# Kernel optimization log

Hardware: AMD Instinct MI355X
Metric: run time of the kernel (lower is better)

## Reference

```python
import jax, jax.numpy as jnp
import numpy as np

N = 50000
E = 800000
IN_FEATS = 128
OUT_FEATS = 16
EDGE_FEATS = 1
NUM_HEADS = 8


def setup_inputs() -> dict:
    key = jax.random.key(0)
    ks = jax.random.split(key, 8)

    def xavier(k, shape):
        fan_in, fan_out = shape[-1], shape[-2] if len(shape) > 1 else shape[-1]
        bound = float(np.sqrt(6.0 / (shape[0] + shape[1])))
        return jax.random.uniform(k, shape, jnp.float32, -bound, bound)

    h = jax.random.normal(ks[0], (N, IN_FEATS), jnp.float32)
    edge_index = jax.random.randint(ks[1], (2, E), 0, N, jnp.int32)
    edge_feat = jax.random.normal(ks[2], (E, EDGE_FEATS), jnp.float32)
    # W_node stored as [in_feats, out_feats*num_heads] so h @ W_node == torch Linear(h)
    W_node = xavier(ks[3], (IN_FEATS, OUT_FEATS * NUM_HEADS))
    W_edge = xavier(ks[4], (EDGE_FEATS, NUM_HEADS))
    a_src = xavier(ks[5], (NUM_HEADS, OUT_FEATS))
    a_dst = xavier(ks[6], (NUM_HEADS, OUT_FEATS))
    return {"h": h, "edge_index": edge_index, "edge_feat": edge_feat,
            "W_node": W_node, "W_edge": W_edge, "a_src": a_src, "a_dst": a_dst}


def reference(h, edge_index, edge_feat, W_node, W_edge, a_src, a_dst):
    n = h.shape[0]
    src, dst = edge_index[0], edge_index[1]
    # node projection: [N, H, F]
    h_trans = (h @ W_node).reshape(n, NUM_HEADS, OUT_FEATS)
    # edge projection: [E, H]
    e_trans = edge_feat @ W_edge
    src_feat = h_trans[src]  # [E, H, F]
    dst_feat = h_trans[dst]  # [E, H, F]
    attn = (src_feat * a_src).sum(-1) + (dst_feat * a_dst).sum(-1) + e_trans  # [E, H]
    attn = jax.nn.leaky_relu(attn, negative_slope=0.2)
    # segment softmax over edges grouped by dst
    max_val = jax.ops.segment_max(attn, dst, num_segments=n)  # [N, H]
    exp_attn = jnp.exp(attn - max_val[dst])
    sum_exp = jax.ops.segment_sum(exp_attn, dst, num_segments=n)  # [N, H]
    alpha = exp_attn / jnp.maximum(sum_exp[dst], 1e-12)  # [E, H]
    msg = src_feat * alpha[..., None]  # [E, H, F]
    out = jax.ops.segment_sum(msg, dst, num_segments=n)  # [N, H, F]
    return out.mean(axis=1)  # [N, F]
```

## Files before the change

kernel.cpp:

```cpp
#include <hip/hip_runtime.h>

#define N_NODES 50000
#define N_EDGES 800000
#define IN_F    128
#define HEADS   8
#define OUT_F   16
#define NB_PROJ 782
#define NB_HIST 3125

typedef unsigned short u16;
typedef __attribute__((ext_vector_type(8))) short bf16x8;
typedef __attribute__((ext_vector_type(4))) float f32x4;

__device__ __forceinline__ float bf2f(u16 u) {
    return __uint_as_float(((unsigned)u) << 16);
}
__device__ __forceinline__ u16 f2bf(float f) {
    unsigned u = __float_as_uint(f);
    unsigned r = 0x7fffu + ((u >> 16) & 1u);
    return (u16)((u + r) >> 16);
}
__device__ __forceinline__ float ldf(const void* p, int i, bool bf) {
    return bf ? bf2f(((const u16*)p)[i]) : ((const float*)p)[i];
}

__global__ void probe_dtype(const void* __restrict__ h, int* __restrict__ flag) {
    if (threadIdx.x == 0 && blockIdx.x == 0) {
        const u16* u = (const u16*)h;
        int cnt = 0;
        for (int i = 0; i < 128; ++i) {
            int e = (u[i] >> 7) & 0xFF;
            if (e >= 90 && e <= 141) cnt++;
        }
        *flag = (cnt >= 110) ? 1 : 0;
    }
}

#define WT_STRIDE 136
__global__ __launch_bounds__(256) void proj_hist(
    const void* __restrict__ h, const void* __restrict__ Wn,
    const void* __restrict__ a_srcp, const void* __restrict__ a_dstp,
    const int* __restrict__ flag, const int* __restrict__ ei,
    u16* __restrict__ ht, float* __restrict__ s_src, float* __restrict__ s_dst,
    int* __restrict__ deg, int* __restrict__ rank)
{
    if (blockIdx.x >= NB_PROJ) {
        int e = (blockIdx.x - NB_PROJ) * 256 + threadIdx.x;
        if (e < N_EDGES) rank[e] = atomicAdd(&deg[ei[N_EDGES + e]], 1);
        return;
    }

    const bool bf = (*flag) != 0;
    __shared__ u16 Wsh[IN_F * WT_STRIDE];
    __shared__ float a_sh[2][IN_F];
    const int tid = threadIdx.x;

    if (tid < 128) a_sh[0][tid] = ldf(a_srcp, tid, bf);
    else           a_sh[1][tid - 128] = ldf(a_dstp, tid - 128, bf);

    {
        const int c8  = (tid & 15) * 8;
        const int kof = tid >> 4;
        const int ksw = (tid & 7) << 3;
        bf16x8 wv[8];
        if (bf) {
            const u16* wp = (const u16*)Wn;
            #pragma unroll
            for (int j = 0; j < 8; ++j)
                wv[j] = *(const bf16x8*)(wp + (size_t)(j * 16 + kof) * IN_F + c8);
        } else {
            const float* wp = (const float*)Wn;
            #pragma unroll
            for (int j = 0; j < 8; ++j) {
                const float* rp = wp + (size_t)(j * 16 + kof) * IN_F + c8;
                float4 fa = *(const float4*)(rp);
                float4 fb = *(const float4*)(rp + 4);
                bf16x8 t;
                t[0] = (short)f2bf(fa.x); t[1] = (short)f2bf(fa.y);
                t[2] = (short)f2bf(fa.z); t[3] = (short)f2bf(fa.w);
                t[4] = (short)f2bf(fb.x); t[5] = (short)f2bf(fb.y);
                t[6] = (short)f2bf(fb.z); t[7] = (short)f2bf(fb.w);
                wv[j] = t;
            }
        }
        #pragma unroll
        for (int j = 0; j < 8; ++j) {
            int kk = (j * 16 + kof) ^ ksw;
            #pragma unroll
            for (int jj = 0; jj < 8; ++jj)
                Wsh[(c8 + jj) * WT_STRIDE + kk] = (u16)wv[j][jj];
        }
    }
    __syncthreads();

    const int wave = tid >> 6, lane = tid & 63;
    const int m = lane & 15, q = lane >> 4;
    const int row_t = blockIdx.x * 64 + wave * 16;

    bf16x8 afr[4];
    int arow = row_t + m;
    if (arow >= N_NODES) arow = N_NODES - 1;
    if (bf) {
        const u16* hp = (const u16*)h + (size_t)arow * IN_F;
        #pragma unroll
        for (int kt = 0; kt < 4; ++kt)
            afr[kt] = *(const bf16x8*)(hp + kt * 32 + q * 8);
    } else {
        const float* hp = (const float*)h + (size_t)arow * IN_F;
        #pragma unroll
        for (int kt = 0; kt < 4; ++kt) {
            bf16x8 t;
            #pragma unroll
            for (int j = 0; j < 8; ++j) t[j] = (short)f2bf(hp[kt * 32 + q * 8 + j]);
            afr[kt] = t;
        }
    }

    f32x4 accs[8];
    #pragma unroll
    for (int ct = 0; ct < 8; ++ct) {
        const int csw = ((2 * ct + (m >> 3)) & 7) << 3;
        f32x4 acc = {0.f, 0.f, 0.f, 0.f};
        #pragma unroll
        for (int kt = 0; kt < 4; ++kt) {
            bf16x8 bfr = *(const bf16x8*)(Wsh + (ct * 16 + m) * WT_STRIDE
                                          + ((kt * 32 + q * 8) ^ csw));
            acc = __builtin_amdgcn_mfma_f32_16x16x32_bf16(afr[kt], bfr, acc, 0, 0, 0);
        }
        accs[ct] = acc;
    }

    __syncthreads();

    const int wbase = wave * 16;
    #pragma unroll
    for (int ct = 0; ct < 8; ++ct)
        #pragma unroll
        for (int r = 0; r < 4; ++r)
            Wsh[(wbase + q * 4 + r) * WT_STRIDE + ct * 16 + m] = f2bf(accs[ct][r]);

    const int r2 = lane & 15, hp2 = lane >> 4;
    const int grow = row_t + r2;
    const u16* wrow = Wsh + (wbase + r2) * WT_STRIDE;
    bf16x8 h0 = *(const bf16x8*)(wrow + hp2 * 32);
    bf16x8 h1 = *(const bf16x8*)(wrow + hp2 * 32 + 8);
    bf16x8 h2 = *(const bf16x8*)(wrow + hp2 * 32 + 16);
    bf16x8 h3 = *(const bf16x8*)(wrow + hp2 * 32 + 24);

    if (grow < N_NODES) {
        u16* hb = ht + (size_t)grow * IN_F + hp2 * 32;
        *(bf16x8*)(hb)      = h0;
        *(bf16x8*)(hb + 8)  = h1;
        *(bf16x8*)(hb + 16) = h2;
        *(bf16x8*)(hb + 24) = h3;
    }

    #pragma unroll
    for (int hh = 0; hh < 2; ++hh) {
        const int hd = hp2 * 2 + hh;
        float s1 = 0.f, s2 = 0.f;
        #pragma unroll
        for (int f = 0; f < 8; ++f) {
            float xa = bf2f((u16)((hh == 0) ? h0[f] : h2[f]));
            float xb = bf2f((u16)((hh == 0) ? h1[f] : h3[f]));
            s1 = fmaf(xa, a_sh[0][hd * 16 + f], s1);
            s1 = fmaf(xb, a_sh[0][hd * 16 + 8 + f], s1);
            s2 = fmaf(xa, a_sh[1][hd * 16 + f], s2);
            s2 = fmaf(xb, a_sh[1][hd * 16 + 8 + f], s2);
        }
        if (grow < N_NODES) {
            s_src[grow * HEADS + hd] = s1;
            s_dst[grow * HEADS + hd] = s2;
        }
    }
}

__global__ __launch_bounds__(1024) void scan_deg(const int* __restrict__ deg,
                                                 int* __restrict__ csr) {
    __shared__ int wsums[16];
    const int tid = threadIdx.x, lane = tid & 63, wid = tid >> 6;
    const int base = tid * 52;

    int s = 0;
    for (int c = 0; c < 13; ++c) {
        int idx = base + c * 4;
        if (idx + 3 < N_NODES) {
            int4 q = *(const int4*)(deg + idx);
            s += q.x + q.y + q.z + q.w;
        } else {
            for (int j = 0; j < 4; ++j)
                if (idx + j < N_NODES) s += deg[idx + j];
        }
    }

    int x = s;
    #pragma unroll
    for (int o = 1; o < 64; o <<= 1) {
        int y = __shfl_up(x, o, 64);
        if (lane >= o) x += y;
    }
    if (lane == 63) wsums[wid] = x;
    __syncthreads();
    if (wid == 0) {
        int v = (lane < 16) ? wsums[lane] : 0;
        #pragma unroll
        for (int o = 1; o < 16; o <<= 1) {
            int y = __shfl_up(v, o, 16);
            if ((lane & 15) >= o) v += y;
        }
        if (lane < 16) wsums[lane] = v;
    }
    __syncthreads();
    int run = ((wid > 0) ? wsums[wid - 1] : 0) + (x - s);

    for (int c = 0; c < 13; ++c) {
        int idx = base + c * 4;
        if (idx + 3 < N_NODES) {
            int4 q = *(const int4*)(deg + idx);
            int4 o4 = {run, run + q.x, run + q.x + q.y, run + q.x + q.y + q.z};
            *(int4*)(csr + idx) = o4;
            run += q.x + q.y + q.z + q.w;
        } else {
            for (int j = 0; j < 4; ++j)
                if (idx + j < N_NODES) { csr[idx + j] = run; run += deg[idx + j]; }
        }
    }
    if (tid == 1023) csr[N_NODES] = run;
}

__global__ __launch_bounds__(256) void scatter_edges(
    const int* __restrict__ ei, const void* __restrict__ ef,
    const int* __restrict__ flag, const int* __restrict__ rank,
    const int* __restrict__ csr, int2* __restrict__ edges)
{
    const bool bf = (*flag) != 0;
    int e = blockIdx.x * 256 + threadIdx.x;
    if (e >= N_EDGES) return;
    int src = ei[e];
    int dst = ei[N_EDGES + e];
    int pos = csr[dst] + rank[e];
    float efv = ldf(ef, e, bf);
    edges[pos] = make_int2(src, __float_as_int(efv));
}

__global__ __launch_bounds__(256) void fused_aggregate(
    const int* __restrict__ csr, const int2* __restrict__ edges,
    const void* __restrict__ We,
    const float* __restrict__ s_src, const float* __restrict__ s_dst,
    const u16* __restrict__ ht, const int* __restrict__ flag,
    void* __restrict__ out)
{
    const bool bf = (*flag) != 0;
    int g = blockIdx.x * 32 + (threadIdx.x >> 3);
    if (g >= N_NODES) return;
    const int hd = threadIdx.x & 7;
    int beg = csr[g], end = csr[g + 1];
    const float dval = s_dst[g * HEADS + hd];
    const float wev = ldf(We, hd, bf);

    float num[16];
    #pragma unroll
    for (int f = 0; f < 16; ++f) num[f] = 0.f;
    float den = 0.f;

    int2 eN = make_int2(0, 0);
    float svN = 0.f;
    bf16x8 v0N = {0,0,0,0,0,0,0,0}, v1N = {0,0,0,0,0,0,0,0};
    if (beg < end) {
        eN = edges[beg];
        svN = s_src[eN.x * HEADS + hd];
        const u16* hp = ht + (size_t)eN.x * IN_F + hd * 16;
        v0N = *(const bf16x8*)hp;
        v1N = *(const bf16x8*)(hp + 8);
    }
    for (int i = beg; i < end; ++i) {
        int2 eC = eN;
        float sv = svN;
        bf16x8 v0 = v0N, v1 = v1N;
        if (i + 1 < end) {
            eN = edges[i + 1];
            svN = s_src[eN.x * HEADS + hd];
            const u16* hp = ht + (size_t)eN.x * IN_F + hd * 16;
            v0N = *(const bf16x8*)hp;
            v1N = *(const bf16x8*)(hp + 8);
        }
        float a = sv + dval + __int_as_float(eC.y) * wev;
        a = (a > 0.f) ? a : 0.2f * a;
        float ex = __expf(a);
        den += ex;
        #pragma unroll
        for (int f = 0; f < 8; ++f) {
            num[f]     = fmaf(ex, bf2f((u16)v0[f]), num[f]);
            num[8 + f] = fmaf(ex, bf2f((u16)v1[f]), num[8 + f]);
        }
    }

    float rc = 1.0f / fmaxf(den, 1e-12f);
    #pragma unroll
    for (int f = 0; f < 16; ++f) num[f] *= rc;
    #pragma unroll
    for (int o = 1; o < 8; o <<= 1)
        #pragma unroll
        for (int f = 0; f < 16; ++f)
            num[f] += __shfl_xor(num[f], o, 8);

    float o0 = num[2 * hd] * 0.125f;
    float o1 = num[2 * hd + 1] * 0.125f;
    if (bf) {
        unsigned pw = ((unsigned)f2bf(o1) << 16) | (unsigned)f2bf(o0);
        *(unsigned*)((u16*)out + (size_t)g * OUT_F + hd * 2) = pw;
    } else {
        float2 f2v = {o0, o1};
        *(float2*)((float*)out + (size_t)g * OUT_F + hd * 2) = f2v;
    }
}

extern "C" void kernel_launch(void* const* d_in, const int* in_sizes, int n_in,
                              void* d_out, int out_size, void* d_ws, size_t ws_size,
                              hipStream_t stream) {
    const void* h     = d_in[0];
    const int*  ei    = (const int*)d_in[1];
    const void* efeat = d_in[2];
    const void* Wn    = d_in[3];
    const void* We    = d_in[4];
    const void* a_src = d_in[5];
    const void* a_dst = d_in[6];

    char* ws = (char*)d_ws;
    int*   flag    = (int*)ws;   ws += 256;
    u16*   ht      = (u16*)ws;   ws += (size_t)N_NODES * IN_F * 2;
    float* s_src   = (float*)ws; ws += (size_t)N_NODES * HEADS * 4;
    float* s_dst   = (float*)ws; ws += (size_t)N_NODES * HEADS * 4;
    int*   deg     = (int*)ws;   ws += (size_t)50048 * 4;
    int*   csr     = (int*)ws;   ws += (size_t)50048 * 4;
    int*   rank    = (int*)ws;   ws += (size_t)N_EDGES * 4;
    int2*  edges   = (int2*)ws;  ws += (size_t)N_EDGES * 8;

    hipLaunchKernelGGL(probe_dtype, dim3(1), dim3(64), 0, stream, h, flag);
    hipMemsetAsync(deg, 0, (size_t)N_NODES * 4, stream);
    hipLaunchKernelGGL(proj_hist, dim3(NB_PROJ + NB_HIST), dim3(256),
                       0, stream, h, Wn, a_src, a_dst, flag, ei,
                       ht, s_src, s_dst, deg, rank);
    hipLaunchKernelGGL(scan_deg, dim3(1), dim3(1024), 0, stream, deg, csr);
    hipLaunchKernelGGL(scatter_edges, dim3((N_EDGES + 255) / 256), dim3(256),
                       0, stream, ei, efeat, flag, rank, csr, edges);
    hipLaunchKernelGGL(fused_aggregate, dim3((N_NODES + 31) / 32), dim3(256),
                       0, stream, csr, edges, We, s_src, s_dst, ht, flag, d_out);
}
```

Measured before the change: 213.1 us.

## Merge scan, scatter and aggregate into one cooperative kernel with grid syncs

Replaces the separate scan, scatter and aggregate kernels with a single cooperative kernel of 512 persistent blocks. Inside it, a two-level parallel scan builds the CSR offsets, then edges are scattered, then nodes are aggregated, with grid.sync between phases. The dtype probe kernel is dropped and each block now detects the dtype itself with a ballot. The aggregate loop is unrolled by four edges to raise the number of gather loads in flight. This removes several launches and the single-block serial scan, in exchange for grid-wide barriers and fewer resident blocks during the aggregation phase.

New measurement: 423.6 us. +98.8%, slower.

```diff
diff --git a/kernel.cpp b/kernel.cpp
--- a/kernel.cpp
+++ b/kernel.cpp
@@ -1,4 +1,7 @@
 #include <hip/hip_runtime.h>
+#include <hip/hip_cooperative_groups.h>
+
+namespace cg = cooperative_groups;
 
 #define N_NODES 50000
 #define N_EDGES 800000
@@ -7,6 +10,10 @@
 #define OUT_F   16
 #define NB_PROJ 782
 #define NB_HIST 3125
+#define NB2     512
+#define GSZ2    (NB2 * 256)
+#define CHUNK   98
+#define NBF     1563
 
 typedef unsigned short u16;
 typedef __attribute__((ext_vector_type(8))) short bf16x8;
@@ -24,23 +31,24 @@
     return bf ? bf2f(((const u16*)p)[i]) : ((const float*)p)[i];
 }
 
-__global__ void probe_dtype(const void* __restrict__ h, int* __restrict__ flag) {
-    if (threadIdx.x == 0 && blockIdx.x == 0) {
+__device__ __forceinline__ bool probe_bf(const void* h, int tid, int* bf_sh) {
+    if (tid < 64) {
         const u16* u = (const u16*)h;
-        int cnt = 0;
-        for (int i = 0; i < 128; ++i) {
-            int e = (u[i] >> 7) & 0xFF;
-            if (e >= 90 && e <= 141) cnt++;
-        }
-        *flag = (cnt >= 110) ? 1 : 0;
-    }
+        int e1 = (u[tid] >> 7) & 0xFF;
+        int e2 = (u[tid + 64] >> 7) & 0xFF;
+        unsigned long long b1 = __ballot(e1 >= 90 && e1 <= 141);
+        unsigned long long b2 = __ballot(e2 >= 90 && e2 <= 141);
+        if (tid == 0) *bf_sh = (__popcll(b1) + __popcll(b2) >= 110) ? 1 : 0;
+    }
+    __syncthreads();
+    return *bf_sh != 0;
 }
 
 #define WT_STRIDE 136
 __global__ __launch_bounds__(256) void proj_hist(
     const void* __restrict__ h, const void* __restrict__ Wn,
     const void* __restrict__ a_srcp, const void* __restrict__ a_dstp,
-    const int* __restrict__ flag, const int* __restrict__ ei,
+    const int* __restrict__ ei,
     u16* __restrict__ ht, float* __restrict__ s_src, float* __restrict__ s_dst,
     int* __restrict__ deg, int* __restrict__ rank)
 {
@@ -50,10 +58,11 @@
         return;
     }
 
-    const bool bf = (*flag) != 0;
     __shared__ u16 Wsh[IN_F * WT_STRIDE];
     __shared__ float a_sh[2][IN_F];
+    __shared__ int bf_sh;
     const int tid = threadIdx.x;
+    const bool bf = probe_bf(h, tid, &bf_sh);
 
     if (tid < 128) a_sh[0][tid] = ldf(a_srcp, tid, bf);
     else           a_sh[1][tid - 128] = ldf(a_dstp, tid - 128, bf);
@@ -91,7 +100,6 @@
                 Wsh[(c8 + jj) * WT_STRIDE + kk] = (u16)wv[j][jj];
         }
     }
-    __syncthreads();
 
     const int wave = tid >> 6, lane = tid & 63;
     const int m = lane & 15, q = lane >> 4;
@@ -115,6 +123,7 @@
             afr[kt] = t;
         }
     }
+    __syncthreads();
 
     f32x4 accs[8];
     #pragma unroll
@@ -129,7 +138,6 @@
         }
         accs[ct] = acc;
     }
-
     __syncthreads();
 
     const int wbase = wave * 16;
@@ -154,7 +162,6 @@
         *(bf16x8*)(hb + 16) = h2;
         *(bf16x8*)(hb + 24) = h3;
     }
-
     #pragma unroll
     for (int hh = 0; hh < 2; ++hh) {
         const int hd = hp2 * 2 + hh;
@@ -175,143 +182,173 @@
     }
 }
 
-__global__ __launch_bounds__(1024) void scan_deg(const int* __restrict__ deg,
-                                                 int* __restrict__ csr) {
-    __shared__ int wsums[16];
-    const int tid = threadIdx.x, lane = tid & 63, wid = tid >> 6;
-    const int base = tid * 52;
-
-    int s = 0;
-    for (int c = 0; c < 13; ++c) {
-        int idx = base + c * 4;
-        if (idx + 3 < N_NODES) {
-            int4 q = *(const int4*)(deg + idx);
-            s += q.x + q.y + q.z + q.w;
-        } else {
-            for (int j = 0; j < 4; ++j)
-                if (idx + j < N_NODES) s += deg[idx + j];
-        }
-    }
-
-    int x = s;
-    #pragma unroll
-    for (int o = 1; o < 64; o <<= 1) {
-        int y = __shfl_up(x, o, 64);
-        if (lane >= o) x += y;
-    }
-    if (lane == 63) wsums[wid] = x;
-    __syncthreads();
-    if (wid == 0) {
-        int v = (lane < 16) ? wsums[lane] : 0;
-        #pragma unroll
-        for (int o = 1; o < 16; o <<= 1) {
-            int y = __shfl_up(v, o, 16);
-            if ((lane & 15) >= o) v += y;
-        }
-        if (lane < 16) wsums[lane] = v;
-    }
-    __syncthreads();
-    int run = ((wid > 0) ? wsums[wid - 1] : 0) + (x - s);
-
-    for (int c = 0; c < 13; ++c) {
-        int idx = base + c * 4;
-        if (idx + 3 < N_NODES) {
-            int4 q = *(const int4*)(deg + idx);
-            int4 o4 = {run, run + q.x, run + q.x + q.y, run + q.x + q.y + q.z};
-            *(int4*)(csr + idx) = o4;
-            run += q.x + q.y + q.z + q.w;
-        } else {
-            for (int j = 0; j < 4; ++j)
-                if (idx + j < N_NODES) { csr[idx + j] = run; run += deg[idx + j]; }
-        }
-    }
-    if (tid == 1023) csr[N_NODES] = run;
-}
-
-__global__ __launch_bounds__(256) void scatter_edges(
-    const int* __restrict__ ei, const void* __restrict__ ef,
-    const int* __restrict__ flag, const int* __restrict__ rank,
-    const int* __restrict__ csr, int2* __restrict__ edges)
-{
-    const bool bf = (*flag) != 0;
-    int e = blockIdx.x * 256 + threadIdx.x;
-    if (e >= N_EDGES) return;
-    int src = ei[e];
-    int dst = ei[N_EDGES + e];
-    int pos = csr[dst] + rank[e];
-    float efv = ldf(ef, e, bf);
-    edges[pos] = make_int2(src, __float_as_int(efv));
-}
-
-__global__ __launch_bounds__(256) void fused_aggregate(
-    const int* __restrict__ csr, const int2* __restrict__ edges,
-    const void* __restrict__ We,
+__global__ __launch_bounds__(256, 2) void coop_tail(
+    const void* __restrict__ h, const int* __restrict__ ei,
+    const void* __restrict__ ef, const void* __restrict__ We,
     const float* __restrict__ s_src, const float* __restrict__ s_dst,
-    const u16* __restrict__ ht, const int* __restrict__ flag,
+    const u16* __restrict__ ht, const int* __restrict__ deg,
+    int* __restrict__ csr, const int* __restrict__ rank,
+    int* __restrict__ partials, int2* __restrict__ edges,
     void* __restrict__ out)
 {
-    const bool bf = (*flag) != 0;
-    int g = blockIdx.x * 32 + (threadIdx.x >> 3);
-    if (g >= N_NODES) return;
-    const int hd = threadIdx.x & 7;
-    int beg = csr[g], end = csr[g + 1];
-    const float dval = s_dst[g * HEADS + hd];
+    cg::grid_group grid = cg::this_grid();
+    __shared__ int wsums[8];
+    __shared__ int bf_sh;
+    const int tid = threadIdx.x, bid = blockIdx.x;
+    const int gtid = bid * 256 + tid;
+    const int lane = tid & 63, wid = tid >> 6;
+    const bool bf = probe_bf(h, tid, &bf_sh);
+
+    {
+        int idx = bid * CHUNK + tid;
+        int v = (tid < CHUNK && idx < N_NODES) ? deg[idx] : 0;
+        #pragma unroll
+        for (int o = 32; o > 0; o >>= 1) v += __shfl_xor(v, o, 64);
+        if (lane == 0) wsums[wid] = v;
+        __syncthreads();
+        if (tid == 0) partials[bid] = wsums[0] + wsums[1] + wsums[2] + wsums[3];
+    }
+    if (gtid == 0) csr[N_NODES] = N_EDGES;
+    grid.sync();
+
+    if (bid == 0) {
+        int p0 = 0, p1 = 0, p2 = 0, p3 = 0, s = 0;
+        if (tid < 128) {
+            p0 = partials[tid * 4];     p1 = partials[tid * 4 + 1];
+            p2 = partials[tid * 4 + 2]; p3 = partials[tid * 4 + 3];
+            s = p0 + p1 + p2 + p3;
+        }
+        int x = s;
+        #pragma unroll
+        for (int o = 1; o < 64; o <<= 1) {
+            int y = __shfl_up(x, o, 64);
+            if (lane >= o) x += y;
+        }
+        if (lane == 63) wsums[wid] = x;
+        __syncthreads();
+        if (tid == 0) { int t0 = wsums[0]; wsums[0] = 0; wsums[1] = t0; }
+        __syncthreads();
+        if (tid < 128) {
+            int run = wsums[wid] + (x - s);
+            partials[tid * 4]     = run; run += p0;
+            partials[tid * 4 + 1] = run; run += p1;
+            partials[tid * 4 + 2] = run; run += p2;
+            partials[tid * 4 + 3] = run;
+        }
+    }
+    grid.sync();
+
+    {
+        int idx = bid * CHUNK + tid;
+        int v = (tid < CHUNK && idx < N_NODES) ? deg[idx] : 0;
+        int x = v;
+        #pragma unroll
+        for (int o = 1; o < 64; o <<= 1) {
+            int y = __shfl_up(x, o, 64);
+            if (lane >= o) x += y;
+        }
+        __syncthreads();
+        if (lane == 63) wsums[wid] = x;
+        __syncthreads();
+        int woff = (wid == 1) ? wsums[0] : 0;
+        if (tid < CHUNK && idx < N_NODES)
+            csr[idx] = partials[bid] + woff + (x - v);
+    }
+    grid.sync();
+
+    for (int e = gtid; e < N_EDGES; e += GSZ2) {
+        int src = ei[e];
+        int dst = ei[N_EDGES + e];
+        int pos = csr[dst] + rank[e];
+        float efv = ldf(ef, e, bf);
+        edges[pos] = make_int2(src, __float_as_int(efv));
+    }
+    grid.sync();
+
+    const int hd = tid & 7;
     const float wev = ldf(We, hd, bf);
-
-    float num[16];
-    #pragma unroll
-    for (int f = 0; f < 16; ++f) num[f] = 0.f;
-    float den = 0.f;
-
-    int2 eN = make_int2(0, 0);
-    float svN = 0.f;
-    bf16x8 v0N = {0,0,0,0,0,0,0,0}, v1N = {0,0,0,0,0,0,0,0};
-    if (beg < end) {
-        eN = edges[beg];
-        svN = s_src[eN.x * HEADS + hd];
-        const u16* hp = ht + (size_t)eN.x * IN_F + hd * 16;
-        v0N = *(const bf16x8*)hp;
-        v1N = *(const bf16x8*)(hp + 8);
-    }
-    for (int i = beg; i < end; ++i) {
-        int2 eC = eN;
-        float sv = svN;
-        bf16x8 v0 = v0N, v1 = v1N;
-        if (i + 1 < end) {
-            eN = edges[i + 1];
-            svN = s_src[eN.x * HEADS + hd];
-            const u16* hp = ht + (size_t)eN.x * IN_F + hd * 16;
-            v0N = *(const bf16x8*)hp;
-            v1N = *(const bf16x8*)(hp + 8);
-        }
-        float a = sv + dval + __int_as_float(eC.y) * wev;
-        a = (a > 0.f) ? a : 0.2f * a;
-        float ex = __expf(a);
-        den += ex;
-        #pragma unroll
-        for (int f = 0; f < 8; ++f) {
-            num[f]     = fmaf(ex, bf2f((u16)v0[f]), num[f]);
-            num[8 + f] = fmaf(ex, bf2f((u16)v1[f]), num[8 + f]);
-        }
-    }
-
-    float rc = 1.0f / fmaxf(den, 1e-12f);
-    #pragma unroll
-    for (int f = 0; f < 16; ++f) num[f] *= rc;
-    #pragma unroll
-    for (int o = 1; o < 8; o <<= 1)
-        #pragma unroll
-        for (int f = 0; f < 16; ++f)
-            num[f] += __shfl_xor(num[f], o, 8);
-
-    float o0 = num[2 * hd] * 0.125f;
-    float o1 = num[2 * hd + 1] * 0.125f;
-    if (bf) {
-        unsigned pw = ((unsigned)f2bf(o1) << 16) | (unsigned)f2bf(o0);
-        *(unsigned*)((u16*)out + (size_t)g * OUT_F + hd * 2) = pw;
-    } else {
-        float2 f2v = {o0, o1};
-        *(float2*)((float*)out + (size_t)g * OUT_F + hd * 2) = f2v;
+    for (int vb = bid; vb < NBF; vb += NB2) {
+        int g = vb * 32 + (tid >> 3);
+        if (g >= N_NODES) continue;
+        int beg = csr[g], end = csr[g + 1];
+        const float dval = s_dst[g * HEADS + hd];
+
+        float num[16];
+        #pragma unroll
+        for (int f = 0; f < 16; ++f) num[f] = 0.f;
+        float den = 0.f;
+
+        int i = beg;
+        for (; i + 4 <= end; i += 4) {
+            int2 ea = edges[i], eb = edges[i + 1], ec = edges[i + 2], ed = edges[i + 3];
+            float sa = s_src[ea.x * HEADS + hd];
+            float sb = s_src[eb.x * HEADS + hd];
+            float sc = s_src[ec.x * HEADS + hd];
+            float sd = s_src[ed.x * HEADS + hd];
+            const u16* pa = ht + (size_t)ea.x * IN_F + hd * 16;
+            const u16* pb = ht + (size_t)eb.x * IN_F + hd * 16;
+            const u16* pc = ht + (size_t)ec.x * IN_F + hd * 16;
+            const u16* pd = ht + (size_t)ed.x * IN_F + hd * 16;
+            bf16x8 va0 = *(const bf16x8*)pa, va1 = *(const bf16x8*)(pa + 8);
+            bf16x8 vb0 = *(const bf16x8*)pb, vb1 = *(const bf16x8*)(pb + 8);
+            bf16x8 vc0 = *(const bf16x8*)pc, vc1 = *(const bf16x8*)(pc + 8);
+            bf16x8 vd0 = *(const bf16x8*)pd, vd1 = *(const bf16x8*)(pd + 8);
+            float aa = sa + dval + __int_as_float(ea.y) * wev;
+            float ab = sb + dval + __int_as_float(eb.y) * wev;
+            float ac = sc + dval + __int_as_float(ec.y) * wev;
+            float ad = sd + dval + __int_as_float(ed.y) * wev;
+            aa = (aa > 0.f) ? aa : 0.2f * aa;
+            ab = (ab > 0.f) ? ab : 0.2f * ab;
+            ac = (ac > 0.f) ? ac : 0.2f * ac;
+            ad = (ad > 0.f) ? ad : 0.2f * ad;
+            float xa = __expf(aa), xb = __expf(ab), xc = __expf(ac), xd = __expf(ad);
+            den += (xa + xb) + (xc + xd);
+            #pragma unroll
+            for (int f = 0; f < 8; ++f) {
+                num[f]     = fmaf(xa, bf2f((u16)va0[f]), num[f]);
+                num[8 + f] = fmaf(xa, bf2f((u16)va1[f]), num[8 + f]);
+                num[f]     = fmaf(xb, bf2f((u16)vb0[f]), num[f]);
+                num[8 + f] = fmaf(xb, bf2f((u16)vb1[f]), num[8 + f]);
+                num[f]     = fmaf(xc, bf2f((u16)vc0[f]), num[f]);
+                num[8 + f] = fmaf(xc, bf2f((u16)vc1[f]), num[8 + f]);
+                num[f]     = fmaf(xd, bf2f((u16)vd0[f]), num[f]);
+                num[8 + f] = fmaf(xd, bf2f((u16)vd1[f]), num[8 + f]);
+            }
+        }
+        for (; i < end; ++i) {
+            int2 eC = edges[i];
+            float sv = s_src[eC.x * HEADS + hd];
+            const u16* hp = ht + (size_t)eC.x * IN_F + hd * 16;
+            bf16x8 v0 = *(const bf16x8*)hp, v1 = *(const bf16x8*)(hp + 8);
+            float a = sv + dval + __int_as_float(eC.y) * wev;
+            a = (a > 0.f) ? a : 0.2f * a;
+            float ex = __expf(a);
+            den += ex;
+            #pragma unroll
+            for (int f = 0; f < 8; ++f) {
+                num[f]     = fmaf(ex, bf2f((u16)v0[f]), num[f]);
+                num[8 + f] = fmaf(ex, bf2f((u16)v1[f]), num[8 + f]);
+            }
+        }
+
+        float rc = 1.0f / fmaxf(den, 1e-12f);
+        #pragma unroll
+        for (int f = 0; f < 16; ++f) num[f] *= rc;
+        #pragma unroll
+        for (int o = 1; o < 8; o <<= 1)
+            #pragma unroll
+            for (int f = 0; f < 16; ++f)
+                num[f] += __shfl_xor(num[f], o, 8);
+
+        float o0 = num[2 * hd] * 0.125f;
+        float o1 = num[2 * hd + 1] * 0.125f;
+        if (bf) {
+            unsigned pw = ((unsigned)f2bf(o1) << 16) | (unsigned)f2bf(o0);
+            *(unsigned*)((u16*)out + (size_t)g * OUT_F + hd * 2) = pw;
+        } else {
+            float2 f2v = {o0, o1};
+            *(float2*)((float*)out + (size_t)g * OUT_F + hd * 2) = f2v;
+        }
     }
 }
 
@@ -327,23 +364,26 @@
     const void* a_dst = d_in[6];
 
     char* ws = (char*)d_ws;
-    int*   flag    = (int*)ws;   ws += 256;
     u16*   ht      = (u16*)ws;   ws += (size_t)N_NODES * IN_F * 2;
-    float* s_src   = (float*)ws; ws += (size_t)N_NODES * HEADS * 4;
-    float* s_dst   = (float*)ws; ws += (size_t)N_NODES * HEADS * 4;
+    float* s_srcp  = (float*)ws; ws += (size_t)N_NODES * HEADS * 4;
+    float* s_dstp  = (float*)ws; ws += (size_t)N_NODES * HEADS * 4;
     int*   deg     = (int*)ws;   ws += (size_t)50048 * 4;
     int*   csr     = (int*)ws;   ws += (size_t)50048 * 4;
     int*   rank    = (int*)ws;   ws += (size_t)N_EDGES * 4;
+    int*   parts   = (int*)ws;   ws += (size_t)1024 * 4;
     int2*  edges   = (int2*)ws;  ws += (size_t)N_EDGES * 8;
 
-    hipLaunchKernelGGL(probe_dtype, dim3(1), dim3(64), 0, stream, h, flag);
     hipMemsetAsync(deg, 0, (size_t)N_NODES * 4, stream);
     hipLaunchKernelGGL(proj_hist, dim3(NB_PROJ + NB_HIST), dim3(256),
-                       0, stream, h, Wn, a_src, a_dst, flag, ei,
-                       ht, s_src, s_dst, deg, rank);
-    hipLaunchKernelGGL(scan_deg, dim3(1), dim3(1024), 0, stream, deg, csr);
-    hipLaunchKernelGGL(scatter_edges, dim3((N_EDGES + 255) / 256), dim3(256),
-                       0, stream, ei, efeat, flag, rank, csr, edges);
-    hipLaunchKernelGGL(fused_aggregate, dim3((N_NODES + 31) / 32), dim3(256),
-                       0, stream, csr, edges, We, s_src, s_dst, ht, flag, d_out);
-}
+                       0, stream, h, Wn, a_src, a_dst, ei,
+                       ht, s_srcp, s_dstp, deg, rank);
+
+    void* out = d_out;
+    void* args[] = {
+        (void*)&h, (void*)&ei, (void*)&efeat, (void*)&We,
+        (void*)&s_srcp, (void*)&s_dstp, (void*)&ht, (void*)&deg,
+        (void*)&csr, (void*)&rank, (void*)&parts, (void*)&edges, (void*)&out
+    };
+    hipLaunchCooperativeKernel(reinterpret_cast<void*>(coop_tail),
+                               dim3(NB2), dim3(256), args, 0, stream);
+}
```
